# Kernel optimization log

Hardware: AMD Instinct MI355X
Metric: run time of the kernel (lower is better)

The kernel has to match this reference:

```python
import jax, jax.numpy as jnp
import numpy as np

N = 20000          # nodes
E = 320000         # edges (avg degree 16)
HID = 256          # hidden_size
HEADS = 8          # num_heads
HD = HID // HEADS  # head_dim = 32


def setup_inputs() -> dict:
    key = jax.random.key(0)
    ks = jax.random.split(key, 12)
    scale = 1.0 / np.sqrt(HID).astype(np.float32)
    def lin_w(k):
        return jax.random.normal(k, (HID, HID), jnp.float32) * scale
    def lin_b(k):
        return jax.random.normal(k, (HID,), jnp.float32) * 0.01
    return {
        "h":   jax.random.normal(ks[0], (N, HID), jnp.float32),
        "Wq": lin_w(ks[1]), "bq": lin_b(ks[2]),
        "Wk": lin_w(ks[3]), "bk": lin_b(ks[4]),
        "Wv": lin_w(ks[5]), "bv": lin_b(ks[6]),
        "Wo": lin_w(ks[7]), "bo": lin_b(ks[8]),
        "rows": jax.random.randint(ks[9],  (E,), 0, N),  # dst/query node of each edge
        "cols": jax.random.randint(ks[10], (E,), 0, N),  # src/key node of each edge
    }


def reference(h, Wq, bq, Wk, bk, Wv, bv, Wo, bo, rows, cols):
    n = h.shape[0]
    scaling = HD ** (-0.5)
    # projections; reshape exactly as torch: (N, head_dim, num_heads)
    q = ((h @ Wq) + bq).reshape(n, HD, HEADS) * scaling
    k = ((h @ Wk) + bk).reshape(n, HD, HEADS)
    v = ((h @ Wv) + bv).reshape(n, HD, HEADS)
    # bsddmm: per-edge, per-head score s[e,h] = sum_d q[rows[e],d,h] * k[cols[e],d,h]
    s = jnp.einsum("edh,edh->eh", q[rows], k[cols])  # [E, HEADS]
    # sparse row-wise softmax (over each row's edges)
    m = jax.ops.segment_max(s, rows, num_segments=n)          # [N, HEADS]
    e = jnp.exp(s - m[rows])                                   # [E, HEADS]
    z = jax.ops.segment_sum(e, rows, num_segments=n)           # [N, HEADS]
    attn = e / z[rows]                                          # [E, HEADS]
    # bspmm: out[i,d,h] = sum_{e: rows[e]=i} attn[e,h] * v[cols[e],d,h]
    out = jax.ops.segment_sum(attn[:, None, :] * v[cols], rows, num_segments=n)  # [N, HD, HEADS]
    return out.reshape(n, -1) @ Wo + bo
```

## Files before the change

### kernel.cpp

```cpp
#include <hip/hip_runtime.h>
#include <hip/hip_bf16.h>
#include <math.h>

#define NNODES 20000
#define NEDGES 320000

using f32x4 = __attribute__((ext_vector_type(4))) float;
using s16x8 = __attribute__((ext_vector_type(8))) short;
using u16x8 = __attribute__((ext_vector_type(8))) unsigned short;

__device__ __forceinline__ float bf2f(unsigned short u) {
    union { unsigned int i; float f; } c; c.i = ((unsigned int)u) << 16; return c.f;
}
__device__ __forceinline__ unsigned short f2bf(float f) {
    __hip_bfloat16 h = __float2bfloat16(f);
    return *reinterpret_cast<unsigned short*>(&h);
}
template <int CTRL>
__device__ __forceinline__ float dpp_xadd(float x) {
    union { float f; int i; } a, b;
    a.f = x;
    b.i = __builtin_amdgcn_update_dpp(0, a.i, CTRL, 0xf, 0xf, true);
    return x + b.f;
}

__global__ __launch_bounds__(256) void prep_all_k(
    const float* __restrict__ Wq, const float* __restrict__ bq,
    const float* __restrict__ Wk, const float* __restrict__ bk,
    const float* __restrict__ Wv, const float* __restrict__ bv,
    const float* __restrict__ Wo, const int* __restrict__ rows,
    const float* __restrict__ h,
    unsigned short* __restrict__ wt, float* __restrict__ bp,
    int* __restrict__ counts, unsigned short* __restrict__ hb)
{
    const int gid = blockIdx.x * 256 + threadIdx.x;
    const float SCQ = 0.17677669529663687f * 1.4426950408889634f;
    if (gid < 262144) {
        const int mat = gid >> 16, r = gid & 65535;
        if (mat < 3) {
            const int k = r >> 8, c = r & 255;
            const int n_old = ((c & 31) << 3) | (c >> 5);
            const float* W = (mat == 0) ? Wq : (mat == 1) ? Wk : Wv;
            float val = W[k * 256 + n_old];
            if (mat == 0) val *= SCQ;
            wt[mat * 65536 + c * 256 + k] = f2bf(val);
        } else {
            const int c = r >> 8, n = r & 255;
            const int n_old = ((c & 31) << 3) | (c >> 5);
            wt[3 * 65536 + n * 256 + c] = f2bf(Wo[n_old * 256 + n]);
        }
    } else if (gid < 262912) {
        const int idx = gid - 262144;
        const int mat = idx >> 8, c = idx & 255;
        const int n_old = ((c & 31) << 3) | (c >> 5);
        const float* b = (mat == 0) ? bq : (mat == 1) ? bk : bv;
        float val = b[n_old];
        if (mat == 0) val *= SCQ;
        bp[mat * 256 + c] = val;
    } else if (gid < 582912) {
        atomicAdd(&counts[rows[gid - 262912]], 1);
    } else {
        const int i = (gid - 582912) * 4;
        const float4 f = *reinterpret_cast<const float4*>(&h[i]);
        ushort4 u;
        u.x = f2bf(f.x); u.y = f2bf(f.y); u.z = f2bf(f.z); u.w = f2bf(f.w);
        *reinterpret_cast<ushort4*>(&hb[i]) = u;
    }
}

__global__ __launch_bounds__(1024) void scan_k(const int* __restrict__ counts,
                                               int* __restrict__ row_start)
{
    __shared__ int wsum[16];
    const int t = threadIdx.x, lane = t & 63, w = t >> 6;
    const int base = t * 20;
    int c[20]; int s = 0;
    #pragma unroll
    for (int j = 0; j < 20; ++j) {
        const int idx = base + j;
        c[j] = (idx < NNODES) ? counts[idx] : 0;
        s += c[j];
    }
    int incl = s;
    #pragma unroll
    for (int off = 1; off < 64; off <<= 1) {
        const int y = __shfl_up(incl, off);
        if (lane >= off) incl += y;
    }
    if (lane == 63) wsum[w] = incl;
    __syncthreads();
    int prev = 0;
    for (int i = 0; i < w; ++i) prev += wsum[i];
    int run = prev + incl - s;
    if (t == 0) row_start[0] = 0;
    #pragma unroll
    for (int j = 0; j < 20; ++j) {
        const int idx = base + j;
        run += c[j];
        if (idx < NNODES) row_start[idx + 1] = run;
    }
}

__global__ void scatter_k(const int* __restrict__ rows, const int* __restrict__ cols,
                          const int* __restrict__ row_start, int* __restrict__ cursor,
                          int* __restrict__ cols_sorted)
{
    const int i = blockIdx.x * blockDim.x + threadIdx.x;
    if (i < NEDGES) {
        const int r = rows[i];
        const int pos = row_start[r] + atomicAdd(&cursor[r], 1);
        cols_sorted[pos] = cols[i];
    }
}

__global__ __launch_bounds__(256) void qkv_mfma_k(
    const unsigned short* __restrict__ hb,
    const unsigned short* __restrict__ wt, const float* __restrict__ bp,
    unsigned short* __restrict__ qo, unsigned short* __restrict__ kv)
{
    const int bm = blockIdx.x * 64;
    const int mat = blockIdx.y >> 1;
    const int bn = (blockIdx.y & 1) * 128;
    const unsigned short* W = wt + mat * 65536;
    const float* bias = bp + mat * 256;

    __shared__ __align__(16) unsigned short As[64][40];
    __shared__ __align__(16) unsigned short Bs[128][40];

    const int t = threadIdx.x;
    const int lane = t & 63, w = t >> 6;
    const int wr = (w >> 1) * 32, wc = (w & 1) * 64;

    f32x4 acc[2][4];
    #pragma unroll
    for (int i = 0; i < 2; ++i)
        #pragma unroll
        for (int j = 0; j < 4; ++j) acc[i][j] = (f32x4){0.f, 0.f, 0.f, 0.f};

    const int arow = t >> 2, koff = (t & 3) * 8;
    const int m0 = min(bm + arow, NNODES - 1);
    const unsigned short* pa  = hb + m0 * 256 + koff;
    const unsigned short* pb0 = W + (bn + arow) * 256 + koff;
    const unsigned short* pb1 = W + (bn + arow + 64) * 256 + koff;

    u16x8 ra  = *(const u16x8*)(pa);
    u16x8 rb0 = *(const u16x8*)(pb0);
    u16x8 rb1 = *(const u16x8*)(pb1);

    #pragma unroll
    for (int kt = 0; kt < 8; ++kt) {
        __syncthreads();
        *(u16x8*)&As[arow][koff]      = ra;
        *(u16x8*)&Bs[arow][koff]      = rb0;
        *(u16x8*)&Bs[arow + 64][koff] = rb1;
        __syncthreads();
        if (kt < 7) {
            const int k0 = (kt + 1) * 32;
            ra  = *(const u16x8*)(pa + k0);
            rb0 = *(const u16x8*)(pb0 + k0);
            rb1 = *(const u16x8*)(pb1 + k0);
        }
        s16x8 a[2], b[4];
        const int kk = (lane >> 4) * 8;
        #pragma unroll
        for (int i = 0; i < 2; ++i)
            a[i] = *(const s16x8*)&As[wr + i * 16 + (lane & 15)][kk];
        #pragma unroll
        for (int j = 0; j < 4; ++j)
            b[j] = *(const s16x8*)&Bs[wc + j * 16 + (lane & 15)][kk];
        #pragma unroll
        for (int i = 0; i < 2; ++i)
            #pragma unroll
            for (int j = 0; j < 4; ++j)
                acc[i][j] = __builtin_amdgcn_mfma_f32_16x16x32_bf16(a[i], b[j], acc[i][j], 0, 0, 0);
    }
    #pragma unroll
    for (int i = 0; i < 2; ++i)
        #pragma unroll
        for (int j = 0; j < 4; ++j) {
            const int n = bn + wc + j * 16 + (lane & 15);
            const float bval = bias[n];
            const int kvbase = ((n >> 3) << 4) + (n & 7) + ((mat == 2) ? 8 : 0);
            #pragma unroll
            for (int r = 0; r < 4; ++r) {
                const int m = bm + wr + i * 16 + (lane >> 4) * 4 + r;
                if (m < NNODES) {
                    const unsigned short val = f2bf(acc[i][j][r] + bval);
                    if (mat == 0) qo[m * 256 + n] = val;
                    else          kv[m * 512 + kvbase] = val;
                }
            }
        }
}

__global__ __launch_bounds__(256) void out_mfma_k(
    const unsigned short* __restrict__ A,
    const unsigned short* __restrict__ wt, const float* __restrict__ bo,
    float* __restrict__ C)
{
    const int bm = blockIdx.x * 64;
    const int bn = blockIdx.y * 128;
    const unsigned short* W = wt + 3 * 65536;

    __shared__ __align__(16) unsigned short As[64][40];
    __shared__ __align__(16) unsigned short Bs[128][40];

    const int t = threadIdx.x;
    const int lane = t & 63, w = t >> 6;
    const int wr = (w >> 1) * 32, wc = (w & 1) * 64;

    f32x4 acc[2][4];
    #pragma unroll
    for (int i = 0; i < 2; ++i)
        #pragma unroll
        for (int j = 0; j < 4; ++j) acc[i][j] = (f32x4){0.f, 0.f, 0.f, 0.f};

    const int arow = t >> 2, koff = (t & 3) * 8;
    const int m0 = min(bm + arow, NNODES - 1);
    const unsigned short* pa  = A + m0 * 256 + koff;
    const unsigned short* pb0 = W + (bn + arow) * 256 + koff;
    const unsigned short* pb1 = W + (bn + arow + 64) * 256 + koff;

    u16x8 ra  = *(const u16x8*)(pa);
    u16x8 rb0 = *(const u16x8*)(pb0);
    u16x8 rb1 = *(const u16x8*)(pb1);

    #pragma unroll
    for (int kt = 0; kt < 8; ++kt) {
        __syncthreads();
        *(u16x8*)&As[arow][koff]      = ra;
        *(u16x8*)&Bs[arow][koff]      = rb0;
        *(u16x8*)&Bs[arow + 64][koff] = rb1;
        __syncthreads();
        if (kt < 7) {
            const int k0 = (kt + 1) * 32;
            ra  = *(const u16x8*)(pa + k0);
            rb0 = *(const u16x8*)(pb0 + k0);
            rb1 = *(const u16x8*)(pb1 + k0);
        }
        s16x8 a[2], b[4];
        const int kk = (lane >> 4) * 8;
        #pragma unroll
        for (int i = 0; i < 2; ++i)
            a[i] = *(const s16x8*)&As[wr + i * 16 + (lane & 15)][kk];
        #pragma unroll
        for (int j = 0; j < 4; ++j)
            b[j] = *(const s16x8*)&Bs[wc + j * 16 + (lane & 15)][kk];
        #pragma unroll
        for (int i = 0; i < 2; ++i)
            #pragma unroll
            for (int j = 0; j < 4; ++j)
                acc[i][j] = __builtin_amdgcn_mfma_f32_16x16x32_bf16(a[i], b[j], acc[i][j], 0, 0, 0);
    }
    #pragma unroll
    for (int i = 0; i < 2; ++i)
        #pragma unroll
        for (int j = 0; j < 4; ++j) {
            const int n = bn + wc + j * 16 + (lane & 15);
            const float bval = bo[n];
            #pragma unroll
            for (int r = 0; r < 4; ++r) {
                const int m = bm + wr + i * 16 + (lane >> 4) * 4 + r;
                if (m < NNODES) C[m * 256 + n] = acc[i][j][r] + bval;
            }
        }
}

__global__ __launch_bounds__(256) void row_attn_k(
    const unsigned short* __restrict__ q, const unsigned short* __restrict__ kv,
    const int* __restrict__ row_start, const int* __restrict__ cols_sorted,
    unsigned short* __restrict__ ot)
{
    const int lane = threadIdx.x & 63;
    const int w5 = lane & 31;
    const int half = lane >> 5;
    const int row = __builtin_amdgcn_readfirstlane(blockIdx.x * 4 + (threadIdx.x >> 6));
    const int rs = row_start[row];
    const int re = row_start[row + 1];
    const int deg = re - rs;

    float qd[8];
    {
        const u16x8 qu = *reinterpret_cast<const u16x8*>(&q[row * 256 + w5 * 8]);
        #pragma unroll
        for (int d = 0; d < 8; ++d) qd[d] = bf2f(qu[d]);
    }
    float o[8] = {0.f, 0.f, 0.f, 0.f, 0.f, 0.f, 0.f, 0.f};
    float z = 0.f;
    const int* cp = cols_sorted + rs;

#define LP(K, V, base) do { \
    const int c0 = cp[min((base), deg - 1)]; \
    const int c1 = cp[min((base) + 1, deg - 1)]; \
    const int cn = half ? c1 : c0; \
    const unsigned short* p_ = kv + cn * 512 + w5 * 16; \
    K = *reinterpret_cast<const u16x8*>(p_); \
    V = *reinterpret_cast<const u16x8*>(p_ + 8); \
} while (0)

#define CMP(K, V, base) do { \
    float pa_ = qd[0] * bf2f(K[0]); \
    float pb_ = qd[1] * bf2f(K[1]); \
    pa_ = fmaf(qd[2], bf2f(K[2]), pa_); \
    pb_ = fmaf(qd[3], bf2f(K[3]), pb_); \
    pa_ = fmaf(qd[4], bf2f(K[4]), pa_); \
    pb_ = fmaf(qd[5], bf2f(K[5]), pb_); \
    pa_ = fmaf(qd[6], bf2f(K[6]), pa_); \
    pb_ = fmaf(qd[7], bf2f(K[7]), pb_); \
    float p_ = pa_ + pb_; \
    p_ = dpp_xadd<0xB1>(p_); \
    p_ = dpp_xadd<0x4E>(p_); \
    const float e_ = ((base) + half < deg) ? exp2f(p_) : 0.f; \
    z += e_; \
    o[0] = fmaf(e_, bf2f(V[0]), o[0]); \
    o[1] = fmaf(e_, bf2f(V[1]), o[1]); \
    o[2] = fmaf(e_, bf2f(V[2]), o[2]); \
    o[3] = fmaf(e_, bf2f(V[3]), o[3]); \
    o[4] = fmaf(e_, bf2f(V[4]), o[4]); \
    o[5] = fmaf(e_, bf2f(V[5]), o[5]); \
    o[6] = fmaf(e_, bf2f(V[6]), o[6]); \
    o[7] = fmaf(e_, bf2f(V[7]), o[7]); \
} while (0)

    if (deg > 0) {
        u16x8 ak0, av0, ak1, av1, bk0, bv0, bk1, bv1;
        LP(ak0, av0, 0);
        LP(ak1, av1, 2);
        for (int i0 = 0; i0 < deg; i0 += 8) {
            const bool hb = (i0 + 4) < deg;
            if (hb) { LP(bk0, bv0, i0 + 4); LP(bk1, bv1, i0 + 6); }
            CMP(ak0, av0, i0);
            CMP(ak1, av1, i0 + 2);
            if (i0 + 8 < deg) { LP(ak0, av0, i0 + 8); LP(ak1, av1, i0 + 10); }
            if (hb) { CMP(bk0, bv0, i0 + 4); CMP(bk1, bv1, i0 + 6); }
        }
    }
#undef LP
#undef CMP

    z += __shfl_xor(z, 32);
    #pragma unroll
    for (int d = 0; d < 8; ++d) o[d] += __shfl_xor(o[d], 32);

    if (half == 0) {
        u16x8 r;
        if (deg > 0) {
            const float iz = 1.0f / z;
            #pragma unroll
            for (int d = 0; d < 8; ++d) r[d] = f2bf(o[d] * iz);
        } else {
            #pragma unroll
            for (int d = 0; d < 8; ++d) r[d] = 0;
        }
        *reinterpret_cast<u16x8*>(&ot[row * 256 + w5 * 8]) = r;
    }
}

extern "C" void kernel_launch(void* const* d_in, const int* in_sizes, int n_in,
                              void* d_out, int out_size, void* d_ws, size_t ws_size,
                              hipStream_t stream)
{
    const float* h  = (const float*)d_in[0];
    const float* Wq = (const float*)d_in[1];
    const float* bq = (const float*)d_in[2];
    const float* Wk = (const float*)d_in[3];
    const float* bk = (const float*)d_in[4];
    const float* Wv = (const float*)d_in[5];
    const float* bv = (const float*)d_in[6];
    const float* Wo = (const float*)d_in[7];
    const float* bo = (const float*)d_in[8];
    const int* rows = (const int*)d_in[9];
    const int* cols = (const int*)d_in[10];
    float* outp = (float*)d_out;

    char* ws = (char*)d_ws;
    unsigned short* q_b  = (unsigned short*)(ws + 0);
    unsigned short* kv_b = (unsigned short*)(ws + 10240000);
    unsigned short* ot_b = (unsigned short*)(ws + 30720000);
    unsigned short* h_b  = (unsigned short*)(ws + 40960000);
    unsigned short* wt   = (unsigned short*)(ws + 51200000);
    float* bp            = (float*)(ws + 51724288);
    int* row_start       = (int*)(ws + 51727360);
    int* counts          = (int*)(ws + 51807488);
    int* cursor          = (int*)(ws + 51887488);
    int* cols_sorted     = (int*)(ws + 51967488);

    hipMemsetAsync(ws + 51807488, 0, 160000, stream);

    prep_all_k<<<7277, 256, 0, stream>>>(Wq, bq, Wk, bk, Wv, bv, Wo, rows, h,
                                         wt, bp, counts, h_b);
    scan_k<<<1, 1024, 0, stream>>>(counts, row_start);
    scatter_k<<<1250, 256, 0, stream>>>(rows, cols, row_start, cursor, cols_sorted);
    qkv_mfma_k<<<dim3(313, 6), 256, 0, stream>>>(h_b, wt, bp, q_b, kv_b);
    row_attn_k<<<5000, 256, 0, stream>>>(q_b, kv_b, row_start, cols_sorted, ot_b);
    out_mfma_k<<<dim3(313, 2), 256, 0, stream>>>(ot_b, wt, bo, outp);
}
```

Baseline: 222.9 us.

## Fuse h conversion into QKV GEMM, merge scatter launch, hold weights in registers

Removes the separate fp32-to-bf16 pass over h. The QKV GEMM now loads fp32 h directly and converts it while staging a full 64x256 A tile in shared memory. The scatter of column indices is folded into the same launch as extra blocks, so one kernel launch goes away and the scatter work can overlap with the GEMM. Both GEMMs now have each wave keep its full 64x256 slice of B in registers and compute the entire output width per block, which drops the per-k-step syncs. The cost is heavy register pressure (128 VGPRs for B plus 64 for accumulators) and fewer, larger blocks, which may lower occupancy.

New measurement: 237.1 us. 1.06x slower.

```diff
diff --git a/kernel.cpp b/kernel.cpp
--- a/kernel.cpp
+++ b/kernel.cpp
@@ -4,6 +4,8 @@
 
 #define NNODES 20000
 #define NEDGES 320000
+#define SCAT_BLOCKS 1250
+#define MBLK 313
 
 using f32x4 = __attribute__((ext_vector_type(4))) float;
 using s16x8 = __attribute__((ext_vector_type(8))) short;
@@ -15,6 +17,11 @@
 __device__ __forceinline__ unsigned short f2bf(float f) {
     __hip_bfloat16 h = __float2bfloat16(f);
     return *reinterpret_cast<unsigned short*>(&h);
+}
+__device__ __forceinline__ u16x8 packA(const float4& x, const float4& y) {
+    u16x8 u; u[0]=f2bf(x.x); u[1]=f2bf(x.y); u[2]=f2bf(x.z); u[3]=f2bf(x.w);
+             u[4]=f2bf(y.x); u[5]=f2bf(y.y); u[6]=f2bf(y.z); u[7]=f2bf(y.w);
+    return u;
 }
 template <int CTRL>
 __device__ __forceinline__ float dpp_xadd(float x) {
@@ -24,14 +31,13 @@
     return x + b.f;
 }
 
-__global__ __launch_bounds__(256) void prep_all_k(
+__global__ __launch_bounds__(256) void prep_hist_k(
     const float* __restrict__ Wq, const float* __restrict__ bq,
     const float* __restrict__ Wk, const float* __restrict__ bk,
     const float* __restrict__ Wv, const float* __restrict__ bv,
     const float* __restrict__ Wo, const int* __restrict__ rows,
-    const float* __restrict__ h,
     unsigned short* __restrict__ wt, float* __restrict__ bp,
-    int* __restrict__ counts, unsigned short* __restrict__ hb)
+    int* __restrict__ counts)
 {
     const int gid = blockIdx.x * 256 + threadIdx.x;
     const float SCQ = 0.17677669529663687f * 1.4426950408889634f;
@@ -57,14 +63,8 @@
         float val = b[n_old];
         if (mat == 0) val *= SCQ;
         bp[mat * 256 + c] = val;
-    } else if (gid < 582912) {
+    } else if (gid < 262912 + NEDGES) {
         atomicAdd(&counts[rows[gid - 262912]], 1);
-    } else {
-        const int i = (gid - 582912) * 4;
-        const float4 f = *reinterpret_cast<const float4*>(&h[i]);
-        ushort4 u;
-        u.x = f2bf(f.x); u.y = f2bf(f.y); u.z = f2bf(f.z); u.w = f2bf(f.w);
-        *reinterpret_cast<ushort4*>(&hb[i]) = u;
     }
 }
 
@@ -101,169 +101,162 @@
     }
 }
 
-__global__ void scatter_k(const int* __restrict__ rows, const int* __restrict__ cols,
-                          const int* __restrict__ row_start, int* __restrict__ cursor,
-                          int* __restrict__ cols_sorted)
-{
-    const int i = blockIdx.x * blockDim.x + threadIdx.x;
-    if (i < NEDGES) {
-        const int r = rows[i];
-        const int pos = row_start[r] + atomicAdd(&cursor[r], 1);
-        cols_sorted[pos] = cols[i];
-    }
-}
-
-__global__ __launch_bounds__(256) void qkv_mfma_k(
-    const unsigned short* __restrict__ hb,
+__global__ __launch_bounds__(256) void qkv_scatter_k(
+    const float* __restrict__ h,
     const unsigned short* __restrict__ wt, const float* __restrict__ bp,
+    const int* __restrict__ rows, const int* __restrict__ cols,
+    const int* __restrict__ row_start, int* __restrict__ cursor,
+    int* __restrict__ cols_sorted,
     unsigned short* __restrict__ qo, unsigned short* __restrict__ kv)
 {
-    const int bm = blockIdx.x * 64;
-    const int mat = blockIdx.y >> 1;
-    const int bn = (blockIdx.y & 1) * 128;
+    const int t = threadIdx.x;
+    if (blockIdx.x < SCAT_BLOCKS) {
+        const int i = blockIdx.x * 256 + t;
+        if (i < NEDGES) {
+            const int r = rows[i];
+            const int pos = row_start[r] + atomicAdd(&cursor[r], 1);
+            cols_sorted[pos] = cols[i];
+        }
+        return;
+    }
+    const int bid = blockIdx.x - SCAT_BLOCKS;
+    const int mat = bid / MBLK;
+    const int bm = (bid % MBLK) * 64;
     const unsigned short* W = wt + mat * 65536;
-    const float* bias = bp + mat * 256;
-
-    __shared__ __align__(16) unsigned short As[64][40];
-    __shared__ __align__(16) unsigned short Bs[128][40];
-
-    const int t = threadIdx.x;
+
+    __shared__ __align__(16) unsigned short As[64][264];
+
     const int lane = t & 63, w = t >> 6;
-    const int wr = (w >> 1) * 32, wc = (w & 1) * 64;
-
-    f32x4 acc[2][4];
-    #pragma unroll
-    for (int i = 0; i < 2; ++i)
+    const int wc = w * 64;
+    const int l15 = lane & 15, l4 = lane >> 4;
+
+    u16x8 breg[4][8];
+    #pragma unroll
+    for (int nt = 0; nt < 4; ++nt)
+        #pragma unroll
+        for (int k8 = 0; k8 < 8; ++k8)
+            breg[nt][k8] = *(const u16x8*)&W[(wc + nt * 16 + l15) * 256 + k8 * 32 + l4 * 8];
+
+    {
+        const int arow = t >> 2, acoff = (t & 3) * 8;
+        const int m0 = min(bm + arow, NNODES - 1);
+        const float* ph = h + m0 * 256 + acoff;
+        #pragma unroll
+        for (int s = 0; s < 8; ++s) {
+            const float4 fa = *(const float4*)(ph + s * 32);
+            const float4 fb = *(const float4*)(ph + s * 32 + 4);
+            *(u16x8*)&As[arow][acoff + s * 32] = packA(fa, fb);
+        }
+    }
+    __syncthreads();
+
+    f32x4 acc[4][4];
+    #pragma unroll
+    for (int i = 0; i < 4; ++i)
         #pragma unroll
         for (int j = 0; j < 4; ++j) acc[i][j] = (f32x4){0.f, 0.f, 0.f, 0.f};
 
-    const int arow = t >> 2, koff = (t & 3) * 8;
-    const int m0 = min(bm + arow, NNODES - 1);
-    const unsigned short* pa  = hb + m0 * 256 + koff;
-    const unsigned short* pb0 = W + (bn + arow) * 256 + koff;
-    const unsigned short* pb1 = W + (bn + arow + 64) * 256 + koff;
-
-    u16x8 ra  = *(const u16x8*)(pa);
-    u16x8 rb0 = *(const u16x8*)(pb0);
-    u16x8 rb1 = *(const u16x8*)(pb1);
-
-    #pragma unroll
-    for (int kt = 0; kt < 8; ++kt) {
-        __syncthreads();
-        *(u16x8*)&As[arow][koff]      = ra;
-        *(u16x8*)&Bs[arow][koff]      = rb0;
-        *(u16x8*)&Bs[arow + 64][koff] = rb1;
-        __syncthreads();
-        if (kt < 7) {
-            const int k0 = (kt + 1) * 32;
-            ra  = *(const u16x8*)(pa + k0);
-            rb0 = *(const u16x8*)(pb0 + k0);
-            rb1 = *(const u16x8*)(pb1 + k0);
-        }
-        s16x8 a[2], b[4];
-        const int kk = (lane >> 4) * 8;
-        #pragma unroll
-        for (int i = 0; i < 2; ++i)
-            a[i] = *(const s16x8*)&As[wr + i * 16 + (lane & 15)][kk];
-        #pragma unroll
-        for (int j = 0; j < 4; ++j)
-            b[j] = *(const s16x8*)&Bs[wc + j * 16 + (lane & 15)][kk];
-        #pragma unroll
-        for (int i = 0; i < 2; ++i)
+    #pragma unroll
+    for (int k8 = 0; k8 < 8; ++k8) {
+        s16x8 a[4];
+        const int kk = k8 * 32 + l4 * 8;
+        #pragma unroll
+        for (int i = 0; i < 4; ++i)
+            a[i] = *(const s16x8*)&As[i * 16 + l15][kk];
+        #pragma unroll
+        for (int i = 0; i < 4; ++i)
             #pragma unroll
             for (int j = 0; j < 4; ++j)
-                acc[i][j] = __builtin_amdgcn_mfma_f32_16x16x32_bf16(a[i], b[j], acc[i][j], 0, 0, 0);
-    }
-    #pragma unroll
-    for (int i = 0; i < 2; ++i)
-        #pragma unroll
-        for (int j = 0; j < 4; ++j) {
-            const int n = bn + wc + j * 16 + (lane & 15);
-            const float bval = bias[n];
-            const int kvbase = ((n >> 3) << 4) + (n & 7) + ((mat == 2) ? 8 : 0);
+                acc[i][j] = __builtin_amdgcn_mfma_f32_16x16x32_bf16(
+                    a[i], (s16x8)breg[j][k8], acc[i][j], 0, 0, 0);
+    }
+
+    #pragma unroll
+    for (int j = 0; j < 4; ++j) {
+        const int n = wc + j * 16 + l15;
+        const float bval = bp[mat * 256 + n];
+        const int kvb = ((n >> 3) << 4) + (n & 7) + ((mat == 2) ? 8 : 0);
+        #pragma unroll
+        for (int i = 0; i < 4; ++i) {
             #pragma unroll
             for (int r = 0; r < 4; ++r) {
-                const int m = bm + wr + i * 16 + (lane >> 4) * 4 + r;
+                const int m = bm + i * 16 + l4 * 4 + r;
                 if (m < NNODES) {
                     const unsigned short val = f2bf(acc[i][j][r] + bval);
                     if (mat == 0) qo[m * 256 + n] = val;
-                    else          kv[m * 512 + kvbase] = val;
+                    else          kv[m * 512 + kvb] = val;
                 }
             }
         }
-}
-
-__global__ __launch_bounds__(256) void out_mfma_k(
+    }
+}
+
+__global__ __launch_bounds__(256) void out_proj_k(
     const unsigned short* __restrict__ A,
     const unsigned short* __restrict__ wt, const float* __restrict__ bo,
     float* __restrict__ C)
 {
+    const int t = threadIdx.x;
     const int bm = blockIdx.x * 64;
-    const int bn = blockIdx.y * 128;
     const unsigned short* W = wt + 3 * 65536;
 
-    __shared__ __align__(16) unsigned short As[64][40];
-    __shared__ __align__(16) unsigned short Bs[128][40];
-
-    const int t = threadIdx.x;
+    __shared__ __align__(16) unsigned short As[64][264];
+
     const int lane = t & 63, w = t >> 6;
-    const int wr = (w >> 1) * 32, wc = (w & 1) * 64;
-
-    f32x4 acc[2][4];
-    #pragma unroll
-    for (int i = 0; i < 2; ++i)
+    const int wc = w * 64;
+    const int l15 = lane & 15, l4 = lane >> 4;
+
+    u16x8 breg[4][8];
+    #pragma unroll
+    for (int nt = 0; nt < 4; ++nt)
+        #pragma unroll
+        for (int k8 = 0; k8 < 8; ++k8)
+            breg[nt][k8] = *(const u16x8*)&W[(wc + nt * 16 + l15) * 256 + k8 * 32 + l4 * 8];
+
+    {
+        const int arow = t >> 2, acoff = (t & 3) * 8;
+        const int m0 = min(bm + arow, NNODES - 1);
+        const unsigned short* pa = A + m0 * 256 + acoff;
+        #pragma unroll
+        for (int s = 0; s < 8; ++s)
+            *(u16x8*)&As[arow][acoff + s * 32] = *(const u16x8*)(pa + s * 32);
+    }
+    __syncthreads();
+
+    f32x4 acc[4][4];
+    #pragma unroll
+    for (int i = 0; i < 4; ++i)
         #pragma unroll
         for (int j = 0; j < 4; ++j) acc[i][j] = (f32x4){0.f, 0.f, 0.f, 0.f};
 
-    const int arow = t >> 2, koff = (t & 3) * 8;
-    const int m0 = min(bm + arow, NNODES - 1);
-    const unsigned short* pa  = A + m0 * 256 + koff;
-    const unsigned short* pb0 = W + (bn + arow) * 256 + koff;
-    const unsigned short* pb1 = W + (bn + arow + 64) * 256 + koff;
-
-    u16x8 ra  = *(const u16x8*)(pa);
-    u16x8 rb0 = *(const u16x8*)(pb0);
-    u16x8 rb1 = *(const u16x8*)(pb1);
-
-    #pragma unroll
-    for (int kt = 0; kt < 8; ++kt) {
-        __syncthreads();
-        *(u16x8*)&As[arow][koff]      = ra;
-        *(u16x8*)&Bs[arow][koff]      = rb0;
-        *(u16x8*)&Bs[arow + 64][koff] = rb1;
-        __syncthreads();
-        if (kt < 7) {
-            const int k0 = (kt + 1) * 32;
-            ra  = *(const u16x8*)(pa + k0);
-            rb0 = *(const u16x8*)(pb0 + k0);
-            rb1 = *(const u16x8*)(pb1 + k0);
-        }
-        s16x8 a[2], b[4];
-        const int kk = (lane >> 4) * 8;
-        #pragma unroll
-        for (int i = 0; i < 2; ++i)
-            a[i] = *(const s16x8*)&As[wr + i * 16 + (lane & 15)][kk];
-        #pragma unroll
-        for (int j = 0; j < 4; ++j)
-            b[j] = *(const s16x8*)&Bs[wc + j * 16 + (lane & 15)][kk];
-        #pragma unroll
-        for (int i = 0; i < 2; ++i)
+    #pragma unroll
+    for (int k8 = 0; k8 < 8; ++k8) {
+        s16x8 a[4];
+        const int kk = k8 * 32 + l4 * 8;
+        #pragma unroll
+        for (int i = 0; i < 4; ++i)
+            a[i] = *(const s16x8*)&As[i * 16 + l15][kk];
+        #pragma unroll
+        for (int i = 0; i < 4; ++i)
             #pragma unroll
             for (int j = 0; j < 4; ++j)
-                acc[i][j] = __builtin_amdgcn_mfma_f32_16x16x32_bf16(a[i], b[j], acc[i][j], 0, 0, 0);
-    }
-    #pragma unroll
-    for (int i = 0; i < 2; ++i)
-        #pragma unroll
-        for (int j = 0; j < 4; ++j) {
-            const int n = bn + wc + j * 16 + (lane & 15);
-            const float bval = bo[n];
+                acc[i][j] = __builtin_amdgcn_mfma_f32_16x16x32_bf16(
+                    a[i], (s16x8)breg[j][k8], acc[i][j], 0, 0, 0);
+    }
+
+    #pragma unroll
+    for (int j = 0; j < 4; ++j) {
+        const int n = wc + j * 16 + l15;
+        const float bval = bo[n];
+        #pragma unroll
+        for (int i = 0; i < 4; ++i) {
             #pragma unroll
             for (int r = 0; r < 4; ++r) {
-                const int m = bm + wr + i * 16 + (lane >> 4) * 4 + r;
+                const int m = bm + i * 16 + l4 * 4 + r;
                 if (m < NNODES) C[m * 256 + n] = acc[i][j][r] + bval;
             }
         }
+    }
 }
 
 __global__ __launch_bounds__(256) void row_attn_k(
@@ -377,21 +370,20 @@
     unsigned short* q_b  = (unsigned short*)(ws + 0);
     unsigned short* kv_b = (unsigned short*)(ws + 10240000);
     unsigned short* ot_b = (unsigned short*)(ws + 30720000);
-    unsigned short* h_b  = (unsigned short*)(ws + 40960000);
-    unsigned short* wt   = (unsigned short*)(ws + 51200000);
-    float* bp            = (float*)(ws + 51724288);
-    int* row_start       = (int*)(ws + 51727360);
-    int* counts          = (int*)(ws + 51807488);
-    int* cursor          = (int*)(ws + 51887488);
-    int* cols_sorted     = (int*)(ws + 51967488);
-
-    hipMemsetAsync(ws + 51807488, 0, 160000, stream);
-
-    prep_all_k<<<7277, 256, 0, stream>>>(Wq, bq, Wk, bk, Wv, bv, Wo, rows, h,
-                                         wt, bp, counts, h_b);
+    unsigned short* wt   = (unsigned short*)(ws + 40960000);
+    float* bp            = (float*)(ws + 41484288);
+    int* row_start       = (int*)(ws + 41487360);
+    int* counts          = (int*)(ws + 41567488);
+    int* cursor          = (int*)(ws + 41647488);
+    int* cols_sorted     = (int*)(ws + 41727488);
+
+    hipMemsetAsync(ws + 41567488, 0, 160000, stream);
+
+    prep_hist_k<<<2277, 256, 0, stream>>>(Wq, bq, Wk, bk, Wv, bv, Wo, rows,
+                                          wt, bp, counts);
     scan_k<<<1, 1024, 0, stream>>>(counts, row_start);
-    scatter_k<<<1250, 256, 0, stream>>>(rows, cols, row_start, cursor, cols_sorted);
-    qkv_mfma_k<<<dim3(313, 6), 256, 0, stream>>>(h_b, wt, bp, q_b, kv_b);
+    qkv_scatter_k<<<SCAT_BLOCKS + 3 * MBLK, 256, 0, stream>>>(
+        h, wt, bp, rows, cols, row_start, cursor, cols_sorted, q_b, kv_b);
     row_attn_k<<<5000, 256, 0, stream>>>(q_b, kv_b, row_start, cols_sorted, ot_b);
-    out_mfma_k<<<dim3(313, 2), 256, 0, stream>>>(ot_b, wt, bo, outp);
-}
+    out_proj_k<<<MBLK, 256, 0, stream>>>(ot_b, wt, bo, outp);
+}
```
